# Kernel tuning notes

Measured on AMD Instinct MI355X. Metric: run time of the kernel, lower is better.

Reference implementation:

```python
import jax, jax.numpy as jnp
import numpy as np


def setup_inputs() -> dict:
    key = jax.random.key(0)
    k1, k2 = jax.random.split(key)
    B, H, N, D = 4, 16, 2048, 64
    x = jax.random.normal(k1, (B, H, N, D), dtype=jnp.float32)
    wqkv = 0.02 * jax.random.normal(k2, (H, D, 3 * D), dtype=jnp.float32)
    bqkv = jnp.zeros((H, 1, 3 * D), dtype=jnp.float32)
    return {"x": x, "wqkv": wqkv, "bqkv": bqkv}


def reference(x, wqkv, bqkv):
    # x: [B, H, N, D]; wqkv: [H, D, 3D]; bqkv: [H, 1, 3D]
    B, H, N, D = x.shape
    scale = D ** (-0.5)
    qkv = jnp.einsum('bhnd,hde->bhne', x, wqkv) + bqkv  # [B,H,N,3D]
    # Faithful to torch: reshape (3D,) -> (D, 3) then unbind last axis,
    # i.e. q/k/v are interleaved (stride-3) columns of the projection.
    qkv = qkv.reshape(B, H, N, D, 3)
    q = qkv[..., 0] * scale
    k = qkv[..., 1]
    v = qkv[..., 2]
    attn = jnp.einsum('bhqd,bhkd->bhqk', q, k)  # [B,H,N,N]
    attn = jax.nn.softmax(attn, axis=-1)
    out = jnp.einsum('bhqk,bhkd->bhqd', attn, v)  # [B,H,N,D]
    return out
```

## Files before the change

### kernel.cpp

```cpp
#include <hip/hip_runtime.h>
#include <hip/hip_bf16.h>
#include <stdint.h>

typedef short bf16x8 __attribute__((ext_vector_type(8)));
typedef short bf16x4 __attribute__((ext_vector_type(4)));
typedef float f32x4 __attribute__((ext_vector_type(4)));

#define BHC 64
#define NQ 2048
#define DD 64
#define NE 192
#define LDP 72
#define WPS (64 * LDP + 8)
#define PLP 36
#define QSCALE 0.1803368801111245f

__device__ __forceinline__ short f2bf(float f) {
  unsigned u = __float_as_uint(f);
  unsigned r = (u + 0x7FFFu + ((u >> 16) & 1u)) >> 16;
  return (short)r;
}

__device__ __forceinline__ bf16x8 pack8(float4 a, float4 b) {
  bf16x8 v;
  v[0] = f2bf(a.x); v[1] = f2bf(a.y); v[2] = f2bf(a.z); v[3] = f2bf(a.w);
  v[4] = f2bf(b.x); v[5] = f2bf(b.y); v[6] = f2bf(b.z); v[7] = f2bf(b.w);
  return v;
}

__device__ __forceinline__ short2 pk_bf16(float a, float b) {
  __hip_bfloat162 c = __float22bfloat162_rn(make_float2(a, b));
  return *reinterpret_cast<short2*>(&c);
}

__global__ __launch_bounds__(256, 4) void proj_kernel(
    const float* __restrict__ x, const float* __restrict__ w,
    const float* __restrict__ bq, short* __restrict__ Qg,
    short* __restrict__ Kg, short* __restrict__ Vtg) {
  __shared__ short wt[3 * WPS];
  __shared__ short sV[4][64 * 24];

  const int tid = threadIdx.x;
  const int bh = blockIdx.x >> 5;
  const int rb = blockIdx.x & 31;
  const int h = bh & 15;

  const float* whp = w + (size_t)h * DD * NE;
  for (int i = 0; i < 48; ++i) {
    int idx = i * 256 + tid;
    int d = idx / NE, e = idx - d * NE;
    int dd = e / 3, wh = e - dd * 3;
    wt[wh * WPS + dd * LDP + d] = f2bf(whp[idx]);
  }
  __syncthreads();

  const int wave = tid >> 6;
  const int lane = tid & 63;
  const int col = lane & 15, quad = lane >> 4;
  const int row0 = rb * 64 + wave * 16;

  const float* xrow = x + ((size_t)bh * NQ + row0 + col) * DD;
  bf16x8 aq[2];
#pragma unroll
  for (int kc = 0; kc < 2; ++kc) {
    const float4* p4 = (const float4*)(xrow + kc * 32 + quad * 8);
    aq[kc] = pack8(p4[0], p4[1]);
  }

  f32x4 acc[12];
#pragma unroll
  for (int nt = 0; nt < 12; ++nt) acc[nt] = (f32x4){0.f, 0.f, 0.f, 0.f};

#pragma unroll
  for (int nt = 0; nt < 12; ++nt) {
    const short* wrow = &wt[(nt >> 2) * WPS + ((nt & 3) * 16 + col) * LDP];
#pragma unroll
    for (int kc = 0; kc < 2; ++kc) {
      bf16x8 bw = *(const bf16x8*)(wrow + kc * 32 + quad * 8);
      acc[nt] = __builtin_amdgcn_mfma_f32_16x16x32_bf16(aq[kc], bw, acc[nt], 0, 0, 0);
    }
  }

  const float* bqh = bq + h * NE;
  short* Qp = Qg + ((size_t)bh * NQ + row0) * DD;
  short* Kp = Kg + ((size_t)bh * NQ + row0) * DD;
  short* sVw = sV[wave];

#pragma unroll
  for (int nt = 0; nt < 12; ++nt) {
    int dd = (nt & 3) * 16 + col;
    float bias = bqh[dd * 3 + (nt >> 2)];
    float v0 = acc[nt][0] + bias, v1 = acc[nt][1] + bias;
    float v2 = acc[nt][2] + bias, v3 = acc[nt][3] + bias;
    if (nt < 4) { v0 *= QSCALE; v1 *= QSCALE; v2 *= QSCALE; v3 *= QSCALE; }
    short2 s01 = pk_bf16(v0, v1);
    short2 s23 = pk_bf16(v2, v3);
    int rowl = quad * 4;
    if (nt < 4) {
      Qp[rowl * DD + dd] = s01.x; Qp[(rowl + 1) * DD + dd] = s01.y;
      Qp[(rowl + 2) * DD + dd] = s23.x; Qp[(rowl + 3) * DD + dd] = s23.y;
    } else if (nt < 8) {
      Kp[rowl * DD + dd] = s01.x; Kp[(rowl + 1) * DD + dd] = s01.y;
      Kp[(rowl + 2) * DD + dd] = s23.x; Kp[(rowl + 3) * DD + dd] = s23.y;
    } else {
      sVw[dd * 24 + rowl] = s01.x; sVw[dd * 24 + rowl + 1] = s01.y;
      sVw[dd * 24 + rowl + 2] = s23.x; sVw[dd * 24 + rowl + 3] = s23.y;
    }
  }

  short* Vp = Vtg + (size_t)bh * DD * NQ + row0;
#pragma unroll
  for (int c = 0; c < 2; ++c) {
    int idx = c * 64 + lane;
    int d = idx >> 1, half = (idx & 1) * 8;
    *(bf16x8*)(Vp + (size_t)d * NQ + half) = *(const bf16x8*)(sVw + d * 24 + half);
  }
}

__global__ __launch_bounds__(256, 2) void attn_kernel(
    const short* __restrict__ Qg, const short* __restrict__ Kg,
    const short* __restrict__ Vtg, float* __restrict__ out) {
  __shared__ short kbuf[2][64 * 64];
  __shared__ short vbuf[2][64 * 64];
  __shared__ short pbuf[4][64 * PLP];

  const int tid = threadIdx.x;
  const int bh = blockIdx.x & 63;
  const int qb = blockIdx.x >> 6;
  const int wave = tid >> 6, lane = tid & 63;
  const int col = lane & 15, quad = lane >> 4;
  const int qbase = qb * 256 + wave * 64;

  bf16x8 bqf[4][2];
#pragma unroll
  for (int ntq = 0; ntq < 4; ++ntq)
#pragma unroll
    for (int kc = 0; kc < 2; ++kc)
      bqf[ntq][kc] = *(const bf16x8*)(Qg + ((size_t)bh * NQ + qbase + ntq * 16 + col) * DD +
                                      kc * 32 + quad * 8);

  bf16x8 onesf;
#pragma unroll
  for (int j = 0; j < 8; ++j) onesf[j] = (short)0x3F80;

  f32x4 o[4][4];
  f32x4 l4[4];
#pragma unroll
  for (int mtq = 0; mtq < 4; ++mtq) {
    l4[mtq] = (f32x4){0.f, 0.f, 0.f, 0.f};
#pragma unroll
    for (int ntd = 0; ntd < 4; ++ntd) o[mtq][ntd] = (f32x4){0.f, 0.f, 0.f, 0.f};
  }

  short* pb = pbuf[wave];
  const short* Kb = Kg + (size_t)bh * NQ * DD;
  const short* Vb = Vtg + (size_t)bh * DD * NQ;

  const int r0 = tid >> 3, c0 = tid & 7;
  const int dst0 = r0 * 64 + ((c0 ^ (r0 & 7)) * 8);
  const int dst1 = (r0 + 32) * 64 + ((c0 ^ (r0 & 7)) * 8);
  const int src0 = r0 * DD + c0 * 8;
  const size_t vsrc0o = (size_t)r0 * NQ + c0 * 8;
  const size_t vsrc1o = (size_t)(r0 + 32) * NQ + c0 * 8;

  {
    bf16x8 k0 = *(const bf16x8*)(Kb + src0);
    bf16x8 k1 = *(const bf16x8*)(Kb + src0 + 32 * DD);
    bf16x8 v0 = *(const bf16x8*)(Vb + vsrc0o);
    bf16x8 v1 = *(const bf16x8*)(Vb + vsrc1o);
    *(bf16x8*)(&kbuf[0][dst0]) = k0;
    *(bf16x8*)(&kbuf[0][dst1]) = k1;
    *(bf16x8*)(&vbuf[0][dst0]) = v0;
    *(bf16x8*)(&vbuf[0][dst1]) = v1;
  }
  __syncthreads();

#pragma unroll 1
  for (int t = 0; t < 32; ++t) {
    const int p = t & 1;
    const short* kb = kbuf[p];
    const short* vb_s = vbuf[p];

    bf16x8 nk0, nk1, nv0, nv1;
    if (t < 31) {
      const short* Kn = Kb + (t + 1) * 64 * DD;
      const short* Vn = Vb + (t + 1) * 64;
      nk0 = *(const bf16x8*)(Kn + src0);
      nk1 = *(const bf16x8*)(Kn + src0 + 32 * DD);
      nv0 = *(const bf16x8*)(Vn + vsrc0o);
      nv1 = *(const bf16x8*)(Vn + vsrc1o);
    }

#pragma unroll
    for (int h = 0; h < 2; ++h) {
#pragma unroll
      for (int j = 0; j < 2; ++j) {
        const int krow = (2 * h + j) * 16 + col;
        const int kx = krow & 7;
        bf16x8 ka0 = *(const bf16x8*)(&kb[krow * 64 + ((quad ^ kx) * 8)]);
        bf16x8 ka1 = *(const bf16x8*)(&kb[krow * 64 + (((4 + quad) ^ kx) * 8)]);
#pragma unroll
        for (int ntq = 0; ntq < 4; ++ntq) {
          f32x4 s = (f32x4){0.f, 0.f, 0.f, 0.f};
          s = __builtin_amdgcn_mfma_f32_16x16x32_bf16(ka0, bqf[ntq][0], s, 0, 0, 0);
          s = __builtin_amdgcn_mfma_f32_16x16x32_bf16(ka1, bqf[ntq][1], s, 0, 0, 0);
          float p0 = __builtin_amdgcn_exp2f(s[0]);
          float p1 = __builtin_amdgcn_exp2f(s[1]);
          float p2 = __builtin_amdgcn_exp2f(s[2]);
          float p3 = __builtin_amdgcn_exp2f(s[3]);
          short2 s01 = pk_bf16(p0, p1);
          short2 s23 = pk_bf16(p2, p3);
          bf16x4 pv; pv[0] = s01.x; pv[1] = s01.y; pv[2] = s23.x; pv[3] = s23.y;
          *(bf16x4*)(&pb[(ntq * 16 + col) * PLP + j * 16 + quad * 4]) = pv;
        }
      }

#pragma unroll
      for (int mtq = 0; mtq < 4; ++mtq) {
        bf16x8 ap = *(const bf16x8*)(&pb[(mtq * 16 + col) * PLP + quad * 8]);
#pragma unroll
        for (int ntd = 0; ntd < 4; ++ntd) {
          const int vrow = ntd * 16 + col;
          bf16x8 vf = *(const bf16x8*)(&vb_s[vrow * 64 + (((h * 4 + quad) ^ (vrow & 7)) * 8)]);
          o[mtq][ntd] = __builtin_amdgcn_mfma_f32_16x16x32_bf16(ap, vf, o[mtq][ntd], 0, 0, 0);
        }
        l4[mtq] = __builtin_amdgcn_mfma_f32_16x16x32_bf16(ap, onesf, l4[mtq], 0, 0, 0);
      }
    }

    if (t < 31) {
      short* kn = kbuf[1 - p];
      short* vn = vbuf[1 - p];
      *(bf16x8*)(&kn[dst0]) = nk0;
      *(bf16x8*)(&kn[dst1]) = nk1;
      *(bf16x8*)(&vn[dst0]) = nv0;
      *(bf16x8*)(&vn[dst1]) = nv1;
      __syncthreads();
    }
  }

#pragma unroll
  for (int mtq = 0; mtq < 4; ++mtq) {
#pragma unroll
    for (int r = 0; r < 4; ++r) {
      float inv = 1.0f / l4[mtq][r];
      int rq = qbase + mtq * 16 + quad * 4 + r;
      float* orow = out + ((size_t)bh * NQ + rq) * DD;
#pragma unroll
      for (int ntd = 0; ntd < 4; ++ntd) orow[ntd * 16 + col] = o[mtq][ntd][r] * inv;
    }
  }
}

extern "C" void kernel_launch(void* const* d_in, const int* in_sizes, int n_in,
                              void* d_out, int out_size, void* d_ws, size_t ws_size,
                              hipStream_t stream) {
  const float* x = (const float*)d_in[0];
  const float* w = (const float*)d_in[1];
  const float* bq = (const float*)d_in[2];
  float* out = (float*)d_out;

  short* Qg = (short*)d_ws;
  short* Kg = Qg + (size_t)BHC * NQ * DD;
  short* Vtg = Kg + (size_t)BHC * NQ * DD;

  proj_kernel<<<dim3(2048), dim3(256), 0, stream>>>(x, w, bq, Qg, Kg, Vtg);
  attn_kernel<<<dim3(512), dim3(256), 0, stream>>>(Qg, Kg, Vtg, out);
}
```

Before: 203.4 us.

## Compute softmax denominator with VALU row sums and process full 64-key P tile

```diff
diff --git a/kernel.cpp b/kernel.cpp
--- a/kernel.cpp
+++ b/kernel.cpp
@@ -12,7 +12,6 @@
 #define NE 192
 #define LDP 72
 #define WPS (64 * LDP + 8)
-#define PLP 36
 #define QSCALE 0.1803368801111245f
 
 __device__ __forceinline__ short f2bf(float f) {
@@ -122,7 +121,7 @@
     const short* __restrict__ Vtg, float* __restrict__ out) {
   __shared__ short kbuf[2][64 * 64];
   __shared__ short vbuf[2][64 * 64];
-  __shared__ short pbuf[4][64 * PLP];
+  __shared__ short pbuf[4][64 * LDP];
 
   const int tid = threadIdx.x;
   const int bh = blockIdx.x & 63;
@@ -139,15 +138,11 @@
       bqf[ntq][kc] = *(const bf16x8*)(Qg + ((size_t)bh * NQ + qbase + ntq * 16 + col) * DD +
                                       kc * 32 + quad * 8);
 
-  bf16x8 onesf;
-#pragma unroll
-  for (int j = 0; j < 8; ++j) onesf[j] = (short)0x3F80;
-
   f32x4 o[4][4];
-  f32x4 l4[4];
+  float l_acc[4];
 #pragma unroll
   for (int mtq = 0; mtq < 4; ++mtq) {
-    l4[mtq] = (f32x4){0.f, 0.f, 0.f, 0.f};
+    l_acc[mtq] = 0.f;
 #pragma unroll
     for (int ntd = 0; ntd < 4; ++ntd) o[mtq][ntd] = (f32x4){0.f, 0.f, 0.f, 0.f};
   }
@@ -192,39 +187,40 @@
     }
 
 #pragma unroll
-    for (int h = 0; h < 2; ++h) {
-#pragma unroll
-      for (int j = 0; j < 2; ++j) {
-        const int krow = (2 * h + j) * 16 + col;
-        const int kx = krow & 7;
-        bf16x8 ka0 = *(const bf16x8*)(&kb[krow * 64 + ((quad ^ kx) * 8)]);
-        bf16x8 ka1 = *(const bf16x8*)(&kb[krow * 64 + (((4 + quad) ^ kx) * 8)]);
-#pragma unroll
-        for (int ntq = 0; ntq < 4; ++ntq) {
-          f32x4 s = (f32x4){0.f, 0.f, 0.f, 0.f};
-          s = __builtin_amdgcn_mfma_f32_16x16x32_bf16(ka0, bqf[ntq][0], s, 0, 0, 0);
-          s = __builtin_amdgcn_mfma_f32_16x16x32_bf16(ka1, bqf[ntq][1], s, 0, 0, 0);
-          float p0 = __builtin_amdgcn_exp2f(s[0]);
-          float p1 = __builtin_amdgcn_exp2f(s[1]);
-          float p2 = __builtin_amdgcn_exp2f(s[2]);
-          float p3 = __builtin_amdgcn_exp2f(s[3]);
-          short2 s01 = pk_bf16(p0, p1);
-          short2 s23 = pk_bf16(p2, p3);
-          bf16x4 pv; pv[0] = s01.x; pv[1] = s01.y; pv[2] = s23.x; pv[3] = s23.y;
-          *(bf16x4*)(&pb[(ntq * 16 + col) * PLP + j * 16 + quad * 4]) = pv;
-        }
+    for (int mtk = 0; mtk < 4; ++mtk) {
+      const int krow = mtk * 16 + col;
+      const int kx = krow & 7;
+      bf16x8 ka0 = *(const bf16x8*)(&kb[krow * 64 + ((quad ^ kx) * 8)]);
+      bf16x8 ka1 = *(const bf16x8*)(&kb[krow * 64 + (((4 + quad) ^ kx) * 8)]);
+#pragma unroll
+      for (int ntq = 0; ntq < 4; ++ntq) {
+        f32x4 s = (f32x4){0.f, 0.f, 0.f, 0.f};
+        s = __builtin_amdgcn_mfma_f32_16x16x32_bf16(ka0, bqf[ntq][0], s, 0, 0, 0);
+        s = __builtin_amdgcn_mfma_f32_16x16x32_bf16(ka1, bqf[ntq][1], s, 0, 0, 0);
+        float p0 = __builtin_amdgcn_exp2f(s[0]);
+        float p1 = __builtin_amdgcn_exp2f(s[1]);
+        float p2 = __builtin_amdgcn_exp2f(s[2]);
+        float p3 = __builtin_amdgcn_exp2f(s[3]);
+        l_acc[ntq] += (p0 + p1) + (p2 + p3);
+        short2 s01 = pk_bf16(p0, p1);
+        short2 s23 = pk_bf16(p2, p3);
+        bf16x4 pv; pv[0] = s01.x; pv[1] = s01.y; pv[2] = s23.x; pv[3] = s23.y;
+        *(bf16x4*)(&pb[(ntq * 16 + col) * LDP + mtk * 16 + quad * 4]) = pv;
       }
-
-#pragma unroll
-      for (int mtq = 0; mtq < 4; ++mtq) {
-        bf16x8 ap = *(const bf16x8*)(&pb[(mtq * 16 + col) * PLP + quad * 8]);
-#pragma unroll
-        for (int ntd = 0; ntd < 4; ++ntd) {
-          const int vrow = ntd * 16 + col;
-          bf16x8 vf = *(const bf16x8*)(&vb_s[vrow * 64 + (((h * 4 + quad) ^ (vrow & 7)) * 8)]);
-          o[mtq][ntd] = __builtin_amdgcn_mfma_f32_16x16x32_bf16(ap, vf, o[mtq][ntd], 0, 0, 0);
-        }
-        l4[mtq] = __builtin_amdgcn_mfma_f32_16x16x32_bf16(ap, onesf, l4[mtq], 0, 0, 0);
+    }
+
+#pragma unroll
+    for (int mtq = 0; mtq < 4; ++mtq) {
+      bf16x8 ap0 = *(const bf16x8*)(&pb[(mtq * 16 + col) * LDP + quad * 8]);
+      bf16x8 ap1 = *(const bf16x8*)(&pb[(mtq * 16 + col) * LDP + 32 + quad * 8]);
+#pragma unroll
+      for (int ntd = 0; ntd < 4; ++ntd) {
+        const int vrow = ntd * 16 + col;
+        const int vx = vrow & 7;
+        bf16x8 vf0 = *(const bf16x8*)(&vb_s[vrow * 64 + ((quad ^ vx) * 8)]);
+        bf16x8 vf1 = *(const bf16x8*)(&vb_s[vrow * 64 + (((4 + quad) ^ vx) * 8)]);
+        o[mtq][ntd] = __builtin_amdgcn_mfma_f32_16x16x32_bf16(ap0, vf0, o[mtq][ntd], 0, 0, 0);
+        o[mtq][ntd] = __builtin_amdgcn_mfma_f32_16x16x32_bf16(ap1, vf1, o[mtq][ntd], 0, 0, 0);
       }
     }
 
@@ -241,9 +237,12 @@
 
 #pragma unroll
   for (int mtq = 0; mtq < 4; ++mtq) {
+    float l = l_acc[mtq];
+    l += __shfl_xor(l, 16);
+    l += __shfl_xor(l, 32);
 #pragma unroll
     for (int r = 0; r < 4; ++r) {
-      float inv = 1.0f / l4[mtq][r];
+      float inv = 1.0f / __shfl(l, quad * 4 + r);
       int rq = qbase + mtq * 16 + quad * 4 + r;
       float* orow = out + ((size_t)bh * NQ + rq) * DD;
 #pragma unroll
```

After: 180.2 us. -11.4%, faster.
